# Kernel optimization log

Measured on AMD Instinct MI355X. Metric: run time of the kernel, lower is better.

## Reference

```python
import jax, jax.numpy as jnp
import numpy as np

D = 1024
H = 8
DK = D // H
DFF = 4 * D
EPS = 1e-6


def layer_norm(x, g, b):
    mu = jnp.mean(x, axis=-1, keepdims=True)
    var = jnp.mean(jnp.square(x - mu), axis=-1, keepdims=True)
    return (x - mu) * jax.lax.rsqrt(var + EPS) * g + b


def setup_inputs() -> dict:
    key = jax.random.key(0)
    ks = jax.random.split(key, 8)
    s = 0.02
    return {
        "x": jax.random.normal(ks[0], (4, 2048, D), dtype=jnp.float32),
        "Wq": jax.random.normal(ks[1], (D, D), dtype=jnp.float32) * s,
        "bq": jnp.zeros((D,), dtype=jnp.float32),
        "Wk": jax.random.normal(ks[2], (D, D), dtype=jnp.float32) * s,
        "bk": jnp.zeros((D,), dtype=jnp.float32),
        "Wv": jax.random.normal(ks[3], (D, D), dtype=jnp.float32) * s,
        "bv": jnp.zeros((D,), dtype=jnp.float32),
        "ln1_g": jnp.ones((D,), dtype=jnp.float32),
        "ln1_b": jnp.zeros((D,), dtype=jnp.float32),
        "W1": jax.random.normal(ks[4], (D, DFF), dtype=jnp.float32) * s,
        "b1": jnp.zeros((DFF,), dtype=jnp.float32),
        "W2": jax.random.normal(ks[5], (DFF, D), dtype=jnp.float32) * s,
        "b2": jnp.zeros((D,), dtype=jnp.float32),
        "ln2_g": jnp.ones((D,), dtype=jnp.float32),
        "ln2_b": jnp.zeros((D,), dtype=jnp.float32),
    }


def reference(x, Wq, bq, Wk, bk, Wv, bv, ln1_g, ln1_b, W1, b1, W2, b2, ln2_g, ln2_b):
    B, S, _ = x.shape

    def split_heads(t):  # [B,S,D] -> [B,H,S,dk]
        return t.reshape(B, S, H, DK).transpose(0, 2, 1, 3)

    Q = split_heads(x @ Wq + bq)
    K = split_heads(x @ Wk + bk)
    V = split_heads(x @ Wv + bv)

    scores = jnp.einsum("bhqd,bhkd->bhqk", Q, K) / jnp.sqrt(jnp.float32(DK))
    attn = jax.nn.softmax(scores, axis=-1)  # dropout is identity at eval
    out = jnp.einsum("bhqk,bhkd->bhqd", attn, V)
    out = out.transpose(0, 2, 1, 3).reshape(B, S, D)
    x1 = layer_norm(out + x, ln1_g, ln1_b)

    h = jax.nn.relu(x1 @ W1 + b1) @ W2 + b2  # dropout identity at eval
    return layer_norm(h + x1, ln2_g, ln2_b)
```

## Files before the change

kernel.cpp:

```cpp
#include <hip/hip_runtime.h>
#include <hip/hip_bf16.h>
#include <stdint.h>

#define D_MODEL 1024
#define NHEADS  8
#define DKH     128
#define DFF     4096
#define SEQ     2048
#define BATCH   4
#define NTOK    (BATCH*SEQ)
#define QKS     2048
#define QSCALE  0.12751743f

typedef float  f32x4  __attribute__((ext_vector_type(4)));
typedef __bf16 bf16x8 __attribute__((ext_vector_type(8)));

static __device__ __forceinline__ float b2f(ushort u) {
    union { uint32_t i; float f; } v; v.i = ((uint32_t)u) << 16; return v.f;
}
static __device__ __forceinline__ ushort f2b(float f) {
    union { float f; uint32_t i; } v; v.f = f;
    uint32_t r = v.i + 0x7fffu + ((v.i >> 16) & 1u);
    return (ushort)(r >> 16);
}
static __device__ __forceinline__ ushort f2b_native(float f) {
    __bf16 h = (__bf16)f;
    return __builtin_bit_cast(ushort, h);
}
static __device__ __forceinline__ float exp2_hw(float x) {
    return __builtin_amdgcn_exp2f(x);
}
static __device__ __forceinline__ void gl_lds16(const void* g, void* l) {
    __builtin_amdgcn_global_load_lds(
        (const __attribute__((address_space(1))) void*)g,
        (__attribute__((address_space(3))) void*)l, 16, 0, 0);
}
static __device__ __forceinline__ float dpp_max16(float x) {
    int t;
    t = __builtin_amdgcn_update_dpp(0, __builtin_bit_cast(int, x), 0xB1, 0xF, 0xF, true);
    x = fmaxf(x, __builtin_bit_cast(float, t));
    t = __builtin_amdgcn_update_dpp(0, __builtin_bit_cast(int, x), 0x4E, 0xF, 0xF, true);
    x = fmaxf(x, __builtin_bit_cast(float, t));
    t = __builtin_amdgcn_update_dpp(0, __builtin_bit_cast(int, x), 0x141, 0xF, 0xF, true);
    x = fmaxf(x, __builtin_bit_cast(float, t));
    t = __builtin_amdgcn_update_dpp(0, __builtin_bit_cast(int, x), 0x140, 0xF, 0xF, true);
    x = fmaxf(x, __builtin_bit_cast(float, t));
    return x;
}

__global__ __launch_bounds__(256) void conv_kernel(
    const float* __restrict__ in, ushort* __restrict__ out, int n)
{
    for (int i = (blockIdx.x * 256 + threadIdx.x) * 4; i < n; i += gridDim.x * 1024) {
        float4 v = *(const float4*)(in + i);
        ushort o[4] = { f2b(v.x), f2b(v.y), f2b(v.z), f2b(v.w) };
        *(uint2*)(out + i) = *(const uint2*)o;
    }
}

__global__ __launch_bounds__(256) void tconv_kernel(
    const float* __restrict__ in, ushort* __restrict__ out, int R, int C)
{
    __shared__ float L[32][33];
    const int tid = threadIdx.x;
    const int tx = tid & 31, ty = tid >> 5;
    const int nbc = C >> 5;
    const int r0 = (blockIdx.x / nbc) << 5;
    const int c0 = (blockIdx.x % nbc) << 5;
    #pragma unroll
    for (int p = 0; p < 4; ++p)
        L[ty + 8 * p][tx] = in[(size_t)(r0 + ty + 8 * p) * C + c0 + tx];
    __syncthreads();
    #pragma unroll
    for (int p = 0; p < 4; ++p)
        out[(size_t)(c0 + ty + 8 * p) * R + r0 + tx] = f2b(L[tx][ty + 8 * p]);
}

__global__ __launch_bounds__(256) void cat3_kernel(
    const float* __restrict__ a, const float* __restrict__ b,
    const float* __restrict__ c, float* __restrict__ out)
{
    const int i = blockIdx.x * 256 + threadIdx.x;
    out[i] = (i < 1024) ? a[i] : (i < 2048) ? b[i - 1024] : c[i - 2048];
}

template<int MODE>
__global__ __launch_bounds__(256) void gemm_bt(
    const ushort* __restrict__ A, const ushort* __restrict__ Bt,
    const float* __restrict__ bias, ushort* __restrict__ C,
    int M, int N, int K, ushort* __restrict__ vt)
{
    __shared__ __align__(16) ushort As[128 * 32];
    __shared__ __align__(16) ushort Bs[128 * 32];

    const int tid  = threadIdx.x;
    const int w    = tid >> 6;
    const int lane = tid & 63;
    const int l16  = lane & 15;
    const int quad = lane >> 4;

    const int nbn = N >> 7;
    const int m0  = (blockIdx.x / nbn) << 7;
    const int n0  = (blockIdx.x % nbn) << 7;

    const int wm = (w >> 1) << 6;
    const int wn = (w & 1) << 6;

    const int srow = (w << 5) + (lane >> 2);
    const int scol = (lane & 3) << 3;
    const ushort* Ag = A  + (size_t)(m0 + srow) * K + scol;
    const ushort* Bg = Bt + (size_t)(n0 + srow) * K + scol;
    ushort* Asw = &As[(w << 5) * 32];
    ushort* Bsw = &Bs[(w << 5) * 32];

    f32x4 acc[4][4] = {};

    for (int k0 = 0; k0 < K; k0 += 32) {
        __syncthreads();
        gl_lds16(Ag + k0,                  Asw);
        gl_lds16(Ag + k0 + (size_t)16 * K, Asw + 16 * 32);
        gl_lds16(Bg + k0,                  Bsw);
        gl_lds16(Bg + k0 + (size_t)16 * K, Bsw + 16 * 32);
        __syncthreads();

        bf16x8 af[4], bf[4];
        #pragma unroll
        for (int i = 0; i < 4; ++i) {
            af[i] = *(const bf16x8*)&As[(wm + i * 16 + l16) * 32 + (quad << 3)];
            bf[i] = *(const bf16x8*)&Bs[(wn + i * 16 + l16) * 32 + (quad << 3)];
        }
        #pragma unroll
        for (int mt = 0; mt < 4; ++mt)
            #pragma unroll
            for (int nt = 0; nt < 4; ++nt)
                acc[mt][nt] = __builtin_amdgcn_mfma_f32_16x16x32_bf16(
                    af[mt], bf[nt], acc[mt][nt], 0, 0, 0);
    }

    if (MODE == 2 && n0 >= 2048) {
        #pragma unroll
        for (int nt = 0; nt < 4; ++nt) {
            const int n  = n0 + wn + (nt << 4) + l16;
            const int hd = n - 2048;
            const float bv = bias[n];
            const size_t vrow = (size_t)(hd >> 7) * 128 + (hd & 127);
            #pragma unroll
            for (int mt = 0; mt < 4; ++mt) {
                const int m = m0 + wm + (mt << 4) + (quad << 2);
                const size_t row = (size_t)(m >> 11) * 1024 + vrow;
                ushort pk[4];
                #pragma unroll
                for (int r = 0; r < 4; ++r) pk[r] = f2b(acc[mt][nt][r] + bv);
                *(uint2*)(vt + row * SEQ + (m & 2047)) = *(const uint2*)pk;
            }
        }
    } else {
        const int ldc = (MODE == 2) ? QKS : N;
        const float qs = (MODE == 2 && n0 < 1024) ? QSCALE : 1.f;
        #pragma unroll
        for (int nt = 0; nt < 4; ++nt) {
            const int n = n0 + wn + (nt << 4) + l16;
            const float bv = bias[n];
            #pragma unroll
            for (int mt = 0; mt < 4; ++mt) {
                #pragma unroll
                for (int r = 0; r < 4; ++r) {
                    const int m = m0 + wm + (mt << 4) + (quad << 2) + r;
                    float v = acc[mt][nt][r] + bv;
                    if (MODE == 1) v = fmaxf(v, 0.f);
                    if (MODE == 2) v *= qs;
                    C[(size_t)m * ldc + n] = f2b(v);
                }
            }
        }
    }
}

__global__ __launch_bounds__(256) void gemm_bt_sk(
    const ushort* __restrict__ A, const ushort* __restrict__ Bt,
    const float* __restrict__ bias, ushort* __restrict__ C0,
    ushort* __restrict__ C1, int M, int N, int K)
{
    __shared__ __align__(16) ushort As[128 * 32];
    __shared__ __align__(16) ushort Bs[128 * 32];

    const int tiles = (M >> 7) * (N >> 7);
    const int sl  = blockIdx.x / tiles;
    const int tix = blockIdx.x % tiles;
    const int kbeg = sl * (K >> 1);
    const int kend = kbeg + (K >> 1);

    const int tid  = threadIdx.x;
    const int w    = tid >> 6;
    const int lane = tid & 63;
    const int l16  = lane & 15;
    const int quad = lane >> 4;

    const int nbn = N >> 7;
    const int m0  = (tix / nbn) << 7;
    const int n0  = (tix % nbn) << 7;

    const int wm = (w >> 1) << 6;
    const int wn = (w & 1) << 6;

    const int srow = (w << 5) + (lane >> 2);
    const int scol = (lane & 3) << 3;
    const ushort* Ag = A  + (size_t)(m0 + srow) * K + scol;
    const ushort* Bg = Bt + (size_t)(n0 + srow) * K + scol;
    ushort* Asw = &As[(w << 5) * 32];
    ushort* Bsw = &Bs[(w << 5) * 32];

    f32x4 acc[4][4] = {};

    for (int k0 = kbeg; k0 < kend; k0 += 32) {
        __syncthreads();
        gl_lds16(Ag + k0,                  Asw);
        gl_lds16(Ag + k0 + (size_t)16 * K, Asw + 16 * 32);
        gl_lds16(Bg + k0,                  Bsw);
        gl_lds16(Bg + k0 + (size_t)16 * K, Bsw + 16 * 32);
        __syncthreads();

        bf16x8 af[4], bf[4];
        #pragma unroll
        for (int i = 0; i < 4; ++i) {
            af[i] = *(const bf16x8*)&As[(wm + i * 16 + l16) * 32 + (quad << 3)];
            bf[i] = *(const bf16x8*)&Bs[(wn + i * 16 + l16) * 32 + (quad << 3)];
        }
        #pragma unroll
        for (int mt = 0; mt < 4; ++mt)
            #pragma unroll
            for (int nt = 0; nt < 4; ++nt)
                acc[mt][nt] = __builtin_amdgcn_mfma_f32_16x16x32_bf16(
                    af[mt], bf[nt], acc[mt][nt], 0, 0, 0);
    }

    ushort* C = sl ? C1 : C0;
    #pragma unroll
    for (int nt = 0; nt < 4; ++nt) {
        const int n = n0 + wn + (nt << 4) + l16;
        const float bv = sl ? 0.f : bias[n];
        #pragma unroll
        for (int mt = 0; mt < 4; ++mt) {
            #pragma unroll
            for (int r = 0; r < 4; ++r) {
                const int m = m0 + wm + (mt << 4) + (quad << 2) + r;
                C[(size_t)m * N + n] = f2b(acc[mt][nt][r] + bv);
            }
        }
    }
}

__global__ __launch_bounds__(512, 2) void gemm8_relu(
    const ushort* __restrict__ A, const ushort* __restrict__ Bt,
    const float* __restrict__ bias, ushort* __restrict__ C,
    int M, int N, int K)
{
    __shared__ __align__(16) ushort lds[65536];

    const int tid  = threadIdx.x;
    const int w    = tid >> 6;
    const int lane = tid & 63;
    const int l16  = lane & 15;
    const int quad = (lane >> 4) & 3;
    const int wm   = w >> 2;
    const int wn   = w & 3;

    const int nbn = N >> 8;
    const int m0  = (blockIdx.x / nbn) << 8;
    const int n0  = (blockIdx.x % nbn) << 8;

    const int rsub = tid >> 3;
    const int gsw  = (tid & 7) ^ (rsub & 7);
    const ushort* Asrc = A  + (size_t)(m0 + rsub) * K + gsw * 8;
    const ushort* Bsrc = Bt + (size_t)(n0 + rsub) * K + gsw * 8;

    auto issue_half = [&](int p, int kt, int d) {
        const ushort* src;
        int base;
        if (p < 2) { src = Asrc + (size_t)(p * 128) * K;       base = d * 16384 + p * 8192; }
        else       { src = Bsrc + (size_t)((p - 2) * 128) * K; base = 32768 + d * 16384 + (p - 2) * 8192; }
        src += kt * 64;
        gl_lds16(src,                  &lds[base + w * 512]);
        gl_lds16(src + (size_t)64 * K, &lds[base + w * 512 + 4096]);
    };

    f32x4  acc[8][4] = {};
    bf16x8 bfr[4];

    auto phase = [&](int cur, int ks, int mq, bool readB) {
        const int Ab = cur * 16384 + wm * 8192;
        const int Bb = 32768 + cur * 16384 + (wn >> 1) * 8192;
        if (readB) {
            #pragma unroll
            for (int nt = 0; nt < 4; ++nt) {
                const int rB = ((wn & 1) << 6) + nt * 16 + l16;
                const int gB = ((ks << 2) + quad) ^ (rB & 7);
                bfr[nt] = *(const bf16x8*)&lds[Bb + rB * 64 + gB * 8];
            }
        }
        bf16x8 afr[4];
        #pragma unroll
        for (int mt = 0; mt < 4; ++mt) {
            const int rA = mq * 64 + mt * 16 + l16;
            const int gA = ((ks << 2) + quad) ^ (rA & 7);
            afr[mt] = *(const bf16x8*)&lds[Ab + rA * 64 + gA * 8];
        }
        __builtin_amdgcn_s_setprio(1);
        #pragma unroll
        for (int mt = 0; mt < 4; ++mt)
            #pragma unroll
            for (int nt = 0; nt < 4; ++nt)
                acc[mq * 4 + mt][nt] = __builtin_amdgcn_mfma_f32_16x16x32_bf16(
                    afr[mt], bfr[nt], acc[mq * 4 + mt][nt], 0, 0, 0);
        __builtin_amdgcn_s_setprio(0);
    };

    const int NT = K >> 6;

    #pragma unroll
    for (int p = 0; p < 4; ++p) issue_half(p, 0, 0);
    issue_half(0, 1, 1);
    asm volatile("s_waitcnt vmcnt(2)" ::: "memory");
    __builtin_amdgcn_sched_barrier(0);
    __builtin_amdgcn_s_barrier();
    __builtin_amdgcn_sched_barrier(0);

    for (int t = 0; t < NT; ++t) {
        const int  cur = t & 1;
        const bool pf  = (t + 1 < NT);

        if (pf) issue_half(1, t + 1, cur ^ 1);
        phase(cur, 0, 0, true);
        if (pf) issue_half(2, t + 1, cur ^ 1);
        phase(cur, 0, 1, false);
        if (pf) issue_half(3, t + 1, cur ^ 1);
        phase(cur, 1, 0, true);
        phase(cur, 1, 1, false);

        __builtin_amdgcn_sched_barrier(0);
        __builtin_amdgcn_s_barrier();
        __builtin_amdgcn_sched_barrier(0);
        if (pf) {
            if (t + 2 < NT) {
                issue_half(0, t + 2, cur);
                asm volatile("s_waitcnt vmcnt(2)" ::: "memory");
            } else {
                asm volatile("s_waitcnt vmcnt(0)" ::: "memory");
            }
            __builtin_amdgcn_sched_barrier(0);
            __builtin_amdgcn_s_barrier();
            __builtin_amdgcn_sched_barrier(0);
        }
    }
    __builtin_amdgcn_sched_barrier(0);

    #pragma unroll
    for (int nt = 0; nt < 4; ++nt) {
        const int n = n0 + wn * 64 + nt * 16 + l16;
        const float bv = bias[n];
        #pragma unroll
        for (int a = 0; a < 8; ++a) {
            const int mrow = m0 + wm * 128 + (a >> 2) * 64 + (a & 3) * 16 + (quad << 2);
            #pragma unroll
            for (int r = 0; r < 4; ++r) {
                const float v = fmaxf(acc[a][nt][r] + bv, 0.f);
                C[(size_t)(mrow + r) * N + n] = f2b(v);
            }
        }
    }
}

__global__ __launch_bounds__(256) void attn_kernel(
    ushort* __restrict__ qk, const ushort* __restrict__ vt)
{
    __shared__ __align__(16) ushort smem[40960];
    ushort* Ks = smem;
    ushort* Vs = smem + 16384;
    ushort* Ps = smem + 32768;

    const int tid  = threadIdx.x;
    const int w    = tid >> 6;
    const int lane = tid & 63;
    const int l16  = lane & 15;
    const int quad = lane >> 4;

    const int bid = ((blockIdx.x & 7) << 7) + (blockIdx.x >> 3);
    const int qb  = bid & 31;
    const int h   = (bid >> 5) & 7;
    const int b   = bid >> 8;

    ushort* Qp = qk + ((size_t)(b * SEQ + qb * 64)) * QKS + h * DKH;
    const ushort* Kp = qk + ((size_t)(b * SEQ)) * QKS + 1024 + h * DKH;
    const ushort* Vp = vt + ((size_t)((b * 8 + h) * 128)) * SEQ;

    #pragma unroll
    for (int i = 0; i < 4; ++i) {
        const int row = w * 16 + i * 4 + quad;
        const int g = (l16 & 8) | ((l16 & 7) ^ (row & 7));
        gl_lds16(Qp + (size_t)row * QKS + g * 8, Vs + (w * 16 + i * 4) * 128);
    }
    #pragma unroll
    for (int i = 0; i < 8; ++i) {
        const int row = w * 32 + i * 4 + quad;
        const int g = (l16 & 8) | ((l16 & 7) ^ (row & 7));
        gl_lds16(Kp + (size_t)row * QKS + g * 8, Ks + (w * 32 + i * 4) * 128);
    }
    __syncthreads();

    bf16x8 aq[4];
    {
        const int r = w * 16 + l16;
        #pragma unroll
        for (int kq = 0; kq < 4; ++kq) {
            const int gk = kq * 4 + quad;
            const int g = (gk & 8) | ((gk & 7) ^ (r & 7));
            aq[kq] = *(const bf16x8*)&Vs[r * 128 + g * 8];
        }
    }
    __syncthreads();

    #pragma unroll
    for (int i = 0; i < 8; ++i) {
        const int d = w * 32 + i * 4 + quad;
        const int g = (l16 & 8) | ((l16 & 7) ^ (d & 7));
        gl_lds16(Vp + (size_t)d * SEQ + g * 8, Vs + (w * 32 + i * 4) * 128);
    }

    f32x4 o[8] = {};
    float mrun[4], lrun[4];
    #pragma unroll
    for (int r = 0; r < 4; ++r) { mrun[r] = -1e30f; lrun[r] = 0.f; }

    for (int t = 0; t < SEQ / 128; ++t) {
        f32x4 s[8] = {};
        #pragma unroll
        for (int nt = 0; nt < 8; ++nt) {
            const int rk = nt * 16 + l16;
            #pragma unroll
            for (int kq = 0; kq < 4; ++kq) {
                const int gk = kq * 4 + quad;
                const int g = (gk & 8) | ((gk & 7) ^ (rk & 7));
                bf16x8 bk = *(const bf16x8*)&Ks[rk * 128 + g * 8];
                s[nt] = __builtin_amdgcn_mfma_f32_16x16x32_bf16(aq[kq], bk, s[nt], 0, 0, 0);
            }
        }
        __syncthreads();

        if (t + 1 < SEQ / 128) {
            #pragma unroll
            for (int i = 0; i < 8; ++i) {
                const int row = w * 32 + i * 4 + quad;
                const int g = (l16 & 8) | ((l16 & 7) ^ (row & 7));
                gl_lds16(Kp + ((size_t)((t + 1) * 128 + row)) * QKS + g * 8,
                         Ks + (w * 32 + i * 4) * 128);
            }
        }

        float vmax[4];
        #pragma unroll
        for (int r = 0; r < 4; ++r) {
            float v = s[0][r];
            #pragma unroll
            for (int nt = 1; nt < 8; ++nt) v = fmaxf(v, s[nt][r]);
            vmax[r] = dpp_max16(v);
        }
        const int grew = (vmax[0] > mrun[0]) | (vmax[1] > mrun[1]) |
                         (vmax[2] > mrun[2]) | (vmax[3] > mrun[3]);
        if (__any(grew)) {
            #pragma unroll
            for (int r = 0; r < 4; ++r) {
                const float mnew = fmaxf(mrun[r], vmax[r]);
                const float alpha = exp2_hw(mrun[r] - mnew);
                mrun[r] = mnew;
                lrun[r] *= alpha;
                #pragma unroll
                for (int nt8 = 0; nt8 < 8; ++nt8)
                    o[nt8][r] *= alpha;
            }
        }
        #pragma unroll
        for (int nt = 0; nt < 8; ++nt)
            #pragma unroll
            for (int r = 0; r < 4; ++r) {
                const float p = exp2_hw(s[nt][r] - mrun[r]);
                lrun[r] += p;
                const int row = w * 16 + (quad << 2) + r;
                Ps[row * 128 + ((nt * 16 + l16) ^ ((row & 15) << 3))] = f2b_native(p);
            }

        #pragma unroll
        for (int kp = 0; kp < 4; ++kp) {
            const int rowp = w * 16 + l16;
            const int gp = kp * 4 + quad;
            const int gsw = gp ^ (rowp & 15);
            bf16x8 ap = *(const bf16x8*)&Ps[rowp * 128 + gsw * 8];
            #pragma unroll
            for (int nt8 = 0; nt8 < 8; ++nt8) {
                const int d = nt8 * 16 + l16;
                const int gv = (gp & 8) | ((gp & 7) ^ (d & 7));
                bf16x8 bv = *(const bf16x8*)&Vs[d * 128 + gv * 8];
                o[nt8] = __builtin_amdgcn_mfma_f32_16x16x32_bf16(ap, bv, o[nt8], 0, 0, 0);
            }
        }
        __syncthreads();

        if (t + 1 < SEQ / 128) {
            #pragma unroll
            for (int i = 0; i < 8; ++i) {
                const int d = w * 32 + i * 4 + quad;
                const int g = (l16 & 8) | ((l16 & 7) ^ (d & 7));
                gl_lds16(Vp + (size_t)d * SEQ + (t + 1) * 128 + g * 8,
                         Vs + (w * 32 + i * 4) * 128);
            }
        }
    }

    #pragma unroll
    for (int r = 0; r < 4; ++r) {
        float v = lrun[r];
        #pragma unroll
        for (int msk = 1; msk <= 8; msk <<= 1)
            v += __shfl_xor(v, msk, 64);
        lrun[r] = v;
    }
    #pragma unroll
    for (int r = 0; r < 4; ++r) {
        const float inv = 1.f / lrun[r];
        const int row = w * 16 + (quad << 2) + r;
        #pragma unroll
        for (int nt8 = 0; nt8 < 8; ++nt8)
            Qp[(size_t)row * QKS + nt8 * 16 + l16] = f2b_native(o[nt8][r] * inv);
    }
}

__global__ __launch_bounds__(256) void ln_kernel(
    const ushort* __restrict__ a, int astride, const ushort* __restrict__ a2,
    const void* __restrict__ res, int res_f32,
    const float* __restrict__ g, const float* __restrict__ be,
    void* __restrict__ out, int out_f32)
{
    __shared__ float red[8];
    const int row = blockIdx.x;
    const int tid = threadIdx.x;
    const int col = tid * 4;

    ushort av[4];
    *(uint2*)av = *(const uint2*)(a + (size_t)row * astride + col);

    float v[4];
    if (res_f32) {
        float4 rr = *(const float4*)((const float*)res + (size_t)row * D_MODEL + col);
        v[0] = b2f(av[0]) + rr.x; v[1] = b2f(av[1]) + rr.y;
        v[2] = b2f(av[2]) + rr.z; v[3] = b2f(av[3]) + rr.w;
    } else {
        ushort rv[4];
        *(uint2*)rv = *(const uint2*)((const ushort*)res + (size_t)row * D_MODEL + col);
        #pragma unroll
        for (int i = 0; i < 4; ++i) v[i] = b2f(av[i]) + b2f(rv[i]);
    }
    if (a2) {
        ushort bv[4];
        *(uint2*)bv = *(const uint2*)(a2 + (size_t)row * D_MODEL + col);
        #pragma unroll
        for (int i = 0; i < 4; ++i) v[i] += b2f(bv[i]);
    }

    float s = v[0] + v[1] + v[2] + v[3];
    #pragma unroll
    for (int m = 1; m <= 32; m <<= 1) s += __shfl_xor(s, m, 64);
    if ((tid & 63) == 0) red[tid >> 6] = s;
    __syncthreads();
    const float mu = (red[0] + red[1] + red[2] + red[3]) * (1.f / D_MODEL);

    float q = 0.f;
    #pragma unroll
    for (int i = 0; i < 4; ++i) { const float d = v[i] - mu; q += d * d; }
    #pragma unroll
    for (int m = 1; m <= 32; m <<= 1) q += __shfl_xor(q, m, 64);
    if ((tid & 63) == 0) red[4 + (tid >> 6)] = q;
    __syncthreads();
    const float var = (red[4] + red[5] + red[6] + red[7]) * (1.f / D_MODEL);
    const float rstd = rsqrtf(var + 1e-6f);

    float4 gg = *(const float4*)(g + col);
    float4 bb = *(const float4*)(be + col);
    float y[4];
    y[0] = (v[0] - mu) * rstd * gg.x + bb.x;
    y[1] = (v[1] - mu) * rstd * gg.y + bb.y;
    y[2] = (v[2] - mu) * rstd * gg.z + bb.z;
    y[3] = (v[3] - mu) * rstd * gg.w + bb.w;

    if (out_f32) {
        float4 ov; ov.x = y[0]; ov.y = y[1]; ov.z = y[2]; ov.w = y[3];
        *(float4*)((float*)out + (size_t)row * D_MODEL + col) = ov;
    } else {
        ushort ov[4] = { f2b(y[0]), f2b(y[1]), f2b(y[2]), f2b(y[3]) };
        *(uint2*)((ushort*)out + (size_t)row * D_MODEL + col) = *(const uint2*)ov;
    }
}

__global__ __launch_bounds__(256) void sentinel_kernel(float* out, float S, int n) {
    for (int i = blockIdx.x * 256 + threadIdx.x; i < n; i += gridDim.x * 256)
        out[i] = S;
}

extern "C" void kernel_launch(void* const* d_in, const int* in_sizes, int n_in,
                              void* d_out, int out_size, void* d_ws, size_t ws_size,
                              hipStream_t stream)
{
    const float* x   = (const float*)d_in[0];
    const float* Wq  = (const float*)d_in[1];
    const float* bq  = (const float*)d_in[2];
    const float* Wk  = (const float*)d_in[3];
    const float* bk  = (const float*)d_in[4];
    const float* Wv  = (const float*)d_in[5];
    const float* bv  = (const float*)d_in[6];
    const float* g1  = (const float*)d_in[7];
    const float* be1 = (const float*)d_in[8];
    const float* W1  = (const float*)d_in[9];
    const float* b1  = (const float*)d_in[10];
    const float* W2  = (const float*)d_in[11];
    const float* b2  = (const float*)d_in[12];
    const float* g2  = (const float*)d_in[13];
    const float* be2 = (const float*)d_in[14];

    const size_t MB = 1024 * 1024;
    dim3 blk(256);

    if (ws_size < 88 * MB) {
        int k = (int)(ws_size >> 23); if (k > 127) k = 127;
        sentinel_kernel<<<dim3(2048), blk, 0, stream>>>(
            (float*)d_out, 1024.f + 8.f * (float)k, out_size);
        return;
    }

    char* ws = (char*)d_ws;
    ushort* qkb    = (ushort*)(ws);
    ushort* vtb    = (ushort*)(ws + 32 * MB);
    ushort* ffn0   = (ushort*)(ws);
    ushort* ffn1   = (ushort*)(ws + 16 * MB);
    ushort* xb     = (ushort*)(ws + 48 * MB);
    ushort* x1     = (ushort*)(ws + 48 * MB);
    ushort* wqkv_t = (ushort*)(ws + 64 * MB);
    ushort* w1t    = (ushort*)(ws + 70 * MB);
    ushort* w2t    = (ushort*)(ws + 78 * MB);
    float*  bqkv   = (float*) (ws + 86 * MB);
    ushort* hbuf   = (ushort*)d_out;

    conv_kernel<<<dim3(2048), blk, 0, stream>>>(x, xb, NTOK * D_MODEL);
    tconv_kernel<<<dim3(1024), blk, 0, stream>>>(Wq, wqkv_t,               1024, 1024);
    tconv_kernel<<<dim3(1024), blk, 0, stream>>>(Wk, wqkv_t + 1024 * 1024, 1024, 1024);
    tconv_kernel<<<dim3(1024), blk, 0, stream>>>(Wv, wqkv_t + 2048 * 1024, 1024, 1024);
    tconv_kernel<<<dim3(4096), blk, 0, stream>>>(W1, w1t, 1024, 4096);
    tconv_kernel<<<dim3(4096), blk, 0, stream>>>(W2, w2t, 4096, 1024);
    cat3_kernel<<<dim3(12), blk, 0, stream>>>(bq, bk, bv, bqkv);

    gemm_bt<2><<<dim3(64 * 24), blk, 0, stream>>>(xb, wqkv_t, bqkv, qkb,
                                                  NTOK, 3072, D_MODEL, vtb);

    attn_kernel<<<dim3(BATCH * NHEADS * (SEQ / 64)), blk, 0, stream>>>(qkb, vtb);

    ln_kernel<<<dim3(NTOK), blk, 0, stream>>>(qkb, QKS, nullptr, x, 1, g1, be1, x1, 0);

    for (int c = 0; c < 2; ++c) {
        const size_t ro = (size_t)c * 4096;
        gemm8_relu<<<dim3(16 * 16), dim3(512), 0, stream>>>(
            x1 + ro * D_MODEL, w1t, b1, hbuf, 4096, DFF, D_MODEL);
        gemm_bt_sk<<<dim3(2 * 32 * 8), blk, 0, stream>>>(
            hbuf, w2t, b2, ffn0 + ro * D_MODEL, ffn1 + ro * D_MODEL,
            4096, D_MODEL, DFF);
    }

    ln_kernel<<<dim3(NTOK), blk, 0, stream>>>(ffn0, D_MODEL, ffn1, x1, 0,
                                              g2, be2, d_out, 1);
}
```

Baseline: 570.4 us.

## Replace QKV and FFN2 GEMMs with double-buffered 128x256 swizzled-LDS kernel

Replaces the simple single-buffered 128x128 GEMMs for the QKV projection and the split-K FFN down-projection with a new 512-thread 128x256-tile kernel. The new kernel uses double-buffered LDS with XOR-swizzled layout, staggered async global-to-LDS prefetch of the next K-tile interleaved with MFMA phases, setprio around MFMA, and an XCD-aware block remapping. It aims to hide global load latency and raise data reuse per tile, at the cost of 96KB LDS per block and fewer blocks in the grid.

Measured after the change: 511.3 us. 1.12x faster.

```diff
diff --git a/kernel.cpp b/kernel.cpp
--- a/kernel.cpp
+++ b/kernel.cpp
@@ -84,172 +84,6 @@
     out[i] = (i < 1024) ? a[i] : (i < 2048) ? b[i - 1024] : c[i - 2048];
 }
 
-template<int MODE>
-__global__ __launch_bounds__(256) void gemm_bt(
-    const ushort* __restrict__ A, const ushort* __restrict__ Bt,
-    const float* __restrict__ bias, ushort* __restrict__ C,
-    int M, int N, int K, ushort* __restrict__ vt)
-{
-    __shared__ __align__(16) ushort As[128 * 32];
-    __shared__ __align__(16) ushort Bs[128 * 32];
-
-    const int tid  = threadIdx.x;
-    const int w    = tid >> 6;
-    const int lane = tid & 63;
-    const int l16  = lane & 15;
-    const int quad = lane >> 4;
-
-    const int nbn = N >> 7;
-    const int m0  = (blockIdx.x / nbn) << 7;
-    const int n0  = (blockIdx.x % nbn) << 7;
-
-    const int wm = (w >> 1) << 6;
-    const int wn = (w & 1) << 6;
-
-    const int srow = (w << 5) + (lane >> 2);
-    const int scol = (lane & 3) << 3;
-    const ushort* Ag = A  + (size_t)(m0 + srow) * K + scol;
-    const ushort* Bg = Bt + (size_t)(n0 + srow) * K + scol;
-    ushort* Asw = &As[(w << 5) * 32];
-    ushort* Bsw = &Bs[(w << 5) * 32];
-
-    f32x4 acc[4][4] = {};
-
-    for (int k0 = 0; k0 < K; k0 += 32) {
-        __syncthreads();
-        gl_lds16(Ag + k0,                  Asw);
-        gl_lds16(Ag + k0 + (size_t)16 * K, Asw + 16 * 32);
-        gl_lds16(Bg + k0,                  Bsw);
-        gl_lds16(Bg + k0 + (size_t)16 * K, Bsw + 16 * 32);
-        __syncthreads();
-
-        bf16x8 af[4], bf[4];
-        #pragma unroll
-        for (int i = 0; i < 4; ++i) {
-            af[i] = *(const bf16x8*)&As[(wm + i * 16 + l16) * 32 + (quad << 3)];
-            bf[i] = *(const bf16x8*)&Bs[(wn + i * 16 + l16) * 32 + (quad << 3)];
-        }
-        #pragma unroll
-        for (int mt = 0; mt < 4; ++mt)
-            #pragma unroll
-            for (int nt = 0; nt < 4; ++nt)
-                acc[mt][nt] = __builtin_amdgcn_mfma_f32_16x16x32_bf16(
-                    af[mt], bf[nt], acc[mt][nt], 0, 0, 0);
-    }
-
-    if (MODE == 2 && n0 >= 2048) {
-        #pragma unroll
-        for (int nt = 0; nt < 4; ++nt) {
-            const int n  = n0 + wn + (nt << 4) + l16;
-            const int hd = n - 2048;
-            const float bv = bias[n];
-            const size_t vrow = (size_t)(hd >> 7) * 128 + (hd & 127);
-            #pragma unroll
-            for (int mt = 0; mt < 4; ++mt) {
-                const int m = m0 + wm + (mt << 4) + (quad << 2);
-                const size_t row = (size_t)(m >> 11) * 1024 + vrow;
-                ushort pk[4];
-                #pragma unroll
-                for (int r = 0; r < 4; ++r) pk[r] = f2b(acc[mt][nt][r] + bv);
-                *(uint2*)(vt + row * SEQ + (m & 2047)) = *(const uint2*)pk;
-            }
-        }
-    } else {
-        const int ldc = (MODE == 2) ? QKS : N;
-        const float qs = (MODE == 2 && n0 < 1024) ? QSCALE : 1.f;
-        #pragma unroll
-        for (int nt = 0; nt < 4; ++nt) {
-            const int n = n0 + wn + (nt << 4) + l16;
-            const float bv = bias[n];
-            #pragma unroll
-            for (int mt = 0; mt < 4; ++mt) {
-                #pragma unroll
-                for (int r = 0; r < 4; ++r) {
-                    const int m = m0 + wm + (mt << 4) + (quad << 2) + r;
-                    float v = acc[mt][nt][r] + bv;
-                    if (MODE == 1) v = fmaxf(v, 0.f);
-                    if (MODE == 2) v *= qs;
-                    C[(size_t)m * ldc + n] = f2b(v);
-                }
-            }
-        }
-    }
-}
-
-__global__ __launch_bounds__(256) void gemm_bt_sk(
-    const ushort* __restrict__ A, const ushort* __restrict__ Bt,
-    const float* __restrict__ bias, ushort* __restrict__ C0,
-    ushort* __restrict__ C1, int M, int N, int K)
-{
-    __shared__ __align__(16) ushort As[128 * 32];
-    __shared__ __align__(16) ushort Bs[128 * 32];
-
-    const int tiles = (M >> 7) * (N >> 7);
-    const int sl  = blockIdx.x / tiles;
-    const int tix = blockIdx.x % tiles;
-    const int kbeg = sl * (K >> 1);
-    const int kend = kbeg + (K >> 1);
-
-    const int tid  = threadIdx.x;
-    const int w    = tid >> 6;
-    const int lane = tid & 63;
-    const int l16  = lane & 15;
-    const int quad = lane >> 4;
-
-    const int nbn = N >> 7;
-    const int m0  = (tix / nbn) << 7;
-    const int n0  = (tix % nbn) << 7;
-
-    const int wm = (w >> 1) << 6;
-    const int wn = (w & 1) << 6;
-
-    const int srow = (w << 5) + (lane >> 2);
-    const int scol = (lane & 3) << 3;
-    const ushort* Ag = A  + (size_t)(m0 + srow) * K + scol;
-    const ushort* Bg = Bt + (size_t)(n0 + srow) * K + scol;
-    ushort* Asw = &As[(w << 5) * 32];
-    ushort* Bsw = &Bs[(w << 5) * 32];
-
-    f32x4 acc[4][4] = {};
-
-    for (int k0 = kbeg; k0 < kend; k0 += 32) {
-        __syncthreads();
-        gl_lds16(Ag + k0,                  Asw);
-        gl_lds16(Ag + k0 + (size_t)16 * K, Asw + 16 * 32);
-        gl_lds16(Bg + k0,                  Bsw);
-        gl_lds16(Bg + k0 + (size_t)16 * K, Bsw + 16 * 32);
-        __syncthreads();
-
-        bf16x8 af[4], bf[4];
-        #pragma unroll
-        for (int i = 0; i < 4; ++i) {
-            af[i] = *(const bf16x8*)&As[(wm + i * 16 + l16) * 32 + (quad << 3)];
-            bf[i] = *(const bf16x8*)&Bs[(wn + i * 16 + l16) * 32 + (quad << 3)];
-        }
-        #pragma unroll
-        for (int mt = 0; mt < 4; ++mt)
-            #pragma unroll
-            for (int nt = 0; nt < 4; ++nt)
-                acc[mt][nt] = __builtin_amdgcn_mfma_f32_16x16x32_bf16(
-                    af[mt], bf[nt], acc[mt][nt], 0, 0, 0);
-    }
-
-    ushort* C = sl ? C1 : C0;
-    #pragma unroll
-    for (int nt = 0; nt < 4; ++nt) {
-        const int n = n0 + wn + (nt << 4) + l16;
-        const float bv = sl ? 0.f : bias[n];
-        #pragma unroll
-        for (int mt = 0; mt < 4; ++mt) {
-            #pragma unroll
-            for (int r = 0; r < 4; ++r) {
-                const int m = m0 + wm + (mt << 4) + (quad << 2) + r;
-                C[(size_t)m * N + n] = f2b(acc[mt][nt][r] + bv);
-            }
-        }
-    }
-}
-
 __global__ __launch_bounds__(512, 2) void gemm8_relu(
     const ushort* __restrict__ A, const ushort* __restrict__ Bt,
     const float* __restrict__ bias, ushort* __restrict__ C,
@@ -370,6 +204,167 @@
     }
 }
 
+template<int MODE>
+__global__ __launch_bounds__(512, 2) void gemm12(
+    const ushort* __restrict__ A, const ushort* __restrict__ Bt,
+    const float* __restrict__ bias, ushort* __restrict__ C,
+    ushort* __restrict__ C2, int M, int N, int K)
+{
+    __shared__ __align__(16) ushort lds[49152];
+
+    const int tid  = threadIdx.x;
+    const int w    = tid >> 6;
+    const int lane = tid & 63;
+    const int l16  = lane & 15;
+    const int quad = (lane >> 4) & 3;
+    const int wm   = w >> 2;
+    const int wn   = w & 3;
+
+    const int cpx  = gridDim.x >> 3;
+    const int bidx = (blockIdx.x & 7) * cpx + (blockIdx.x >> 3);
+
+    int tix = bidx, kbeg = 0, kend = K, sl = 0;
+    if (MODE == 3) {
+        const int tiles = (M >> 7) * (N >> 8);
+        sl   = bidx / tiles;
+        tix  = bidx % tiles;
+        kbeg = sl * (K >> 1);
+        kend = kbeg + (K >> 1);
+    }
+    const int nbn = N >> 8;
+    const int m0  = (tix / nbn) << 7;
+    const int n0  = (tix % nbn) << 8;
+
+    const int rsub = tid >> 3;
+    const int gsw  = (tid & 7) ^ (rsub & 7);
+    const ushort* Asrc = A  + (size_t)(m0 + rsub) * K + gsw * 8 + kbeg;
+    const ushort* Bsrc = Bt + (size_t)(n0 + rsub) * K + gsw * 8 + kbeg;
+
+    auto issue_half = [&](int p, int kt, int d) {
+        const ushort* src;
+        int base;
+        if (p == 0) { src = Asrc;                              base = d * 8192; }
+        else        { src = Bsrc + (size_t)((p - 1) * 128) * K; base = 16384 + d * 16384 + (p - 1) * 8192; }
+        src += kt * 64;
+        gl_lds16(src,                  &lds[base + w * 512]);
+        gl_lds16(src + (size_t)64 * K, &lds[base + w * 512 + 4096]);
+    };
+
+    f32x4 acc[4][4] = {};
+
+    auto phase = [&](int cur, int ks) {
+        const int Ab = cur * 8192;
+        const int Bb = 16384 + cur * 16384;
+        bf16x8 afr[4], bfr[4];
+        #pragma unroll
+        for (int nt = 0; nt < 4; ++nt) {
+            const int rB = wn * 64 + nt * 16 + l16;
+            const int gB = ((ks << 2) + quad) ^ (rB & 7);
+            bfr[nt] = *(const bf16x8*)&lds[Bb + rB * 64 + gB * 8];
+        }
+        #pragma unroll
+        for (int mt = 0; mt < 4; ++mt) {
+            const int rA = wm * 64 + mt * 16 + l16;
+            const int gA = ((ks << 2) + quad) ^ (rA & 7);
+            afr[mt] = *(const bf16x8*)&lds[Ab + rA * 64 + gA * 8];
+        }
+        __builtin_amdgcn_s_setprio(1);
+        #pragma unroll
+        for (int mt = 0; mt < 4; ++mt)
+            #pragma unroll
+            for (int nt = 0; nt < 4; ++nt)
+                acc[mt][nt] = __builtin_amdgcn_mfma_f32_16x16x32_bf16(
+                    afr[mt], bfr[nt], acc[mt][nt], 0, 0, 0);
+        __builtin_amdgcn_s_setprio(0);
+    };
+
+    const int NT = (kend - kbeg) >> 6;
+
+    issue_half(0, 0, 0);
+    issue_half(1, 0, 0);
+    issue_half(2, 0, 0);
+    issue_half(0, 1, 1);
+    asm volatile("s_waitcnt vmcnt(2)" ::: "memory");
+    __builtin_amdgcn_sched_barrier(0);
+    __builtin_amdgcn_s_barrier();
+    __builtin_amdgcn_sched_barrier(0);
+
+    for (int t = 0; t < NT; ++t) {
+        const int  cur = t & 1;
+        const bool pf  = (t + 1 < NT);
+
+        if (pf) issue_half(1, t + 1, cur ^ 1);
+        phase(cur, 0);
+        if (pf) issue_half(2, t + 1, cur ^ 1);
+        phase(cur, 1);
+
+        __builtin_amdgcn_sched_barrier(0);
+        __builtin_amdgcn_s_barrier();
+        __builtin_amdgcn_sched_barrier(0);
+        if (pf) {
+            if (t + 2 < NT) {
+                issue_half(0, t + 2, cur);
+                asm volatile("s_waitcnt vmcnt(2)" ::: "memory");
+            } else {
+                asm volatile("s_waitcnt vmcnt(0)" ::: "memory");
+            }
+            __builtin_amdgcn_sched_barrier(0);
+            __builtin_amdgcn_s_barrier();
+            __builtin_amdgcn_sched_barrier(0);
+        }
+    }
+    __builtin_amdgcn_sched_barrier(0);
+
+    if (MODE == 2 && n0 >= 2048) {
+        #pragma unroll
+        for (int nt = 0; nt < 4; ++nt) {
+            const int n  = n0 + wn * 64 + nt * 16 + l16;
+            const int hd = n - 2048;
+            const float bv = bias[n];
+            const size_t vrow = (size_t)(hd >> 7) * 128 + (hd & 127);
+            #pragma unroll
+            for (int mt = 0; mt < 4; ++mt) {
+                const int m = m0 + wm * 64 + mt * 16 + (quad << 2);
+                const size_t row = (size_t)(m >> 11) * 1024 + vrow;
+                ushort pk[4];
+                #pragma unroll
+                for (int r = 0; r < 4; ++r) pk[r] = f2b(acc[mt][nt][r] + bv);
+                *(uint2*)(C2 + row * SEQ + (m & 2047)) = *(const uint2*)pk;
+            }
+        }
+    } else if (MODE == 2) {
+        const float qs = (n0 < 1024) ? QSCALE : 1.f;
+        #pragma unroll
+        for (int nt = 0; nt < 4; ++nt) {
+            const int n = n0 + wn * 64 + nt * 16 + l16;
+            const float bv = bias[n];
+            #pragma unroll
+            for (int mt = 0; mt < 4; ++mt) {
+                #pragma unroll
+                for (int r = 0; r < 4; ++r) {
+                    const int m = m0 + wm * 64 + mt * 16 + (quad << 2) + r;
+                    C[(size_t)m * QKS + n] = f2b((acc[mt][nt][r] + bv) * qs);
+                }
+            }
+        }
+    } else {
+        ushort* Co = sl ? C2 : C;
+        #pragma unroll
+        for (int nt = 0; nt < 4; ++nt) {
+            const int n = n0 + wn * 64 + nt * 16 + l16;
+            const float bv = sl ? 0.f : bias[n];
+            #pragma unroll
+            for (int mt = 0; mt < 4; ++mt) {
+                #pragma unroll
+                for (int r = 0; r < 4; ++r) {
+                    const int m = m0 + wm * 64 + mt * 16 + (quad << 2) + r;
+                    Co[(size_t)m * N + n] = f2b(acc[mt][nt][r] + bv);
+                }
+            }
+        }
+    }
+}
+
 __global__ __launch_bounds__(256) void attn_kernel(
     ushort* __restrict__ qk, const ushort* __restrict__ vt)
 {
@@ -492,8 +487,8 @@
         for (int kp = 0; kp < 4; ++kp) {
             const int rowp = w * 16 + l16;
             const int gp = kp * 4 + quad;
-            const int gsw = gp ^ (rowp & 15);
-            bf16x8 ap = *(const bf16x8*)&Ps[rowp * 128 + gsw * 8];
+            const int gsw2 = gp ^ (rowp & 15);
+            bf16x8 ap = *(const bf16x8*)&Ps[rowp * 128 + gsw2 * 8];
             #pragma unroll
             for (int nt8 = 0; nt8 < 8; ++nt8) {
                 const int d = nt8 * 16 + l16;
@@ -655,8 +650,8 @@
     tconv_kernel<<<dim3(4096), blk, 0, stream>>>(W2, w2t, 4096, 1024);
     cat3_kernel<<<dim3(12), blk, 0, stream>>>(bq, bk, bv, bqkv);
 
-    gemm_bt<2><<<dim3(64 * 24), blk, 0, stream>>>(xb, wqkv_t, bqkv, qkb,
-                                                  NTOK, 3072, D_MODEL, vtb);
+    gemm12<2><<<dim3(64 * 12), dim3(512), 0, stream>>>(
+        xb, wqkv_t, bqkv, qkb, vtb, NTOK, 3072, D_MODEL);
 
     attn_kernel<<<dim3(BATCH * NHEADS * (SEQ / 64)), blk, 0, stream>>>(qkb, vtb);
 
@@ -666,7 +661,7 @@
         const size_t ro = (size_t)c * 4096;
         gemm8_relu<<<dim3(16 * 16), dim3(512), 0, stream>>>(
             x1 + ro * D_MODEL, w1t, b1, hbuf, 4096, DFF, D_MODEL);
-        gemm_bt_sk<<<dim3(2 * 32 * 8), blk, 0, stream>>>(
+        gemm12<3><<<dim3(2 * 32 * 4), dim3(512), 0, stream>>>(
             hbuf, w2t, b2, ffn0 + ro * D_MODEL, ffn1 + ro * D_MODEL,
             4096, D_MODEL, DFF);
     }
```
